# Kernel tuning notes

Measured on AMD Instinct MI355X. Metric: run time of the kernel, lower is better.

Reference implementation:

```python
import jax, jax.numpy as jnp
import numpy as np

N, C, H, W = 8, 128, 40, 40
EMBED, HEADS = 128, 8
HEAD_DIM = EMBED // HEADS  # 16


def setup_inputs() -> dict:
    key = jax.random.key(0)
    k1, k2, k3 = jax.random.split(key, 3)
    x = jax.random.normal(k1, (N, C, H, W), dtype=jnp.float32)
    # 1x1 conv weights collapsed to matrices
    w_qkv = jax.random.normal(k2, (3 * EMBED, C), dtype=jnp.float32) * (1.0 / np.sqrt(C))
    w_o = jax.random.normal(k3, (C, EMBED), dtype=jnp.float32) * (1.0 / np.sqrt(EMBED))
    b_o = jnp.zeros((C,), dtype=jnp.float32)
    return {"x": x, "w_qkv": w_qkv, "w_o": w_o, "b_o": b_o}


def reference(x, w_qkv, w_o, b_o):
    n, c, h, w = x.shape
    s = h * w  # spatial tokens
    # qkv 1x1 conv: (n, 3*embed, h, w) -> (n, heads, 3, head_dim, s)
    qkv = jnp.einsum('nchw,oc->nohw', x, w_qkv)
    qkv = qkv.reshape(n, HEADS, 3, HEAD_DIM, s)
    q, k, v = qkv[:, :, 0], qkv[:, :, 1], qkv[:, :, 2]  # (n, heads, head_dim, s)
    scale = 1.0 / jnp.sqrt(jnp.asarray(HEAD_DIM, dtype=x.dtype))
    # energy[n,h,i,j] = sum_c q[n,h,c,i] * k[n,h,c,j]
    energy = jnp.einsum('nhci,nhcj->nhij', q, k) * scale
    attn = jax.nn.softmax(energy, axis=-1)  # (n, heads, s, s)
    # out[n,h,c,i] = sum_j attn[n,h,i,j] * v[n,h,c,j]
    out = jnp.einsum('nhij,nhcj->nhci', attn, v)
    out = out.reshape(n, HEADS * HEAD_DIM, h, w)
    o = jnp.einsum('nchw,oc->nohw', out, w_o) + b_o[None, :, None, None]
    return o
```

## Files before the change

kernel.cpp:

```cpp
#include <hip/hip_runtime.h>
#include <hip/hip_bf16.h>

#define NB    8
#define CIN   128
#define SLEN  1600
#define HEADS 8
#define HD    16
#define NH    64
#define VCH   17

#define QKV_SUB (NH * HD * SLEN)
#define VB_SUB  (NH * VCH * SLEN)

#define SCALE_Q 0.36067376022224085f

typedef __attribute__((ext_vector_type(8)))  short  short8;
typedef __attribute__((ext_vector_type(16))) float  f32x16;
typedef __attribute__((ext_vector_type(2)))  unsigned uint2v;

__device__ inline unsigned short f2bf(float f) {
    union { float f; unsigned u; } x; x.f = f;
    unsigned r = x.u + 0x7FFFu + ((x.u >> 16) & 1u);
    return (unsigned short)(r >> 16);
}

__device__ inline unsigned pkbf(float a, float b) {
    __hip_bfloat162 h = __float22bfloat162_rn(make_float2(a, b));
    union { __hip_bfloat162 h; unsigned u; } c; c.h = h; return c.u;
}

__device__ inline short8 mk8(unsigned w0, unsigned w1, unsigned w2, unsigned w3) {
    union { unsigned u[4]; short8 s; } t;
    t.u[0] = w0; t.u[1] = w1; t.u[2] = w2; t.u[3] = w3; return t.s;
}

template <int MODE>
__global__ __launch_bounds__(256) void proj_kernel(const float* __restrict__ In,
                                                   const float* __restrict__ W,
                                                   const float* __restrict__ bias,
                                                   float* __restrict__ OutF,
                                                   unsigned short* __restrict__ qT,
                                                   unsigned short* __restrict__ kT,
                                                   unsigned short* __restrict__ vB) {
    __shared__ float Wt[128 * 64];
    __shared__ float Xt[128 * 64];

    const int tid = threadIdx.x;
    const int tx = tid & 15;
    const int ty = tid >> 4;
    const int n = blockIdx.z;
    const int m0 = blockIdx.y * 64;
    const int s0 = blockIdx.x * 64;

    const float4* W4 = (const float4*)W;
#pragma unroll
    for (int it = 0; it < 8; ++it) {
        int idx = tid + it * 256;
        int m = idx & 63;
        int k4 = idx >> 6;
        float4 wv = W4[(m0 + m) * 32 + k4];
        Wt[(k4 * 4 + 0) * 64 + m] = wv.x;
        Wt[(k4 * 4 + 1) * 64 + m] = wv.y;
        Wt[(k4 * 4 + 2) * 64 + m] = wv.z;
        Wt[(k4 * 4 + 3) * 64 + m] = wv.w;
    }
    const float4* X4 = (const float4*)In;
    float4* Xt4 = (float4*)Xt;
#pragma unroll
    for (int it = 0; it < 8; ++it) {
        int idx = tid + it * 256;
        int k = idx >> 4;
        int s4 = idx & 15;
        Xt4[k * 16 + s4] = X4[(n * CIN + k) * 400 + (s0 >> 2) + s4];
    }
    __syncthreads();

    const float4* Wt4 = (const float4*)Wt;
    const float4* Xt4r = (const float4*)Xt;
    float acc[4][4];
#pragma unroll
    for (int i = 0; i < 4; ++i)
#pragma unroll
        for (int j = 0; j < 4; ++j) acc[i][j] = 0.f;

#pragma unroll 4
    for (int k = 0; k < 128; ++k) {
        float4 a = Wt4[k * 16 + ty];
        float4 b = Xt4r[k * 16 + tx];
        float af[4] = {a.x, a.y, a.z, a.w};
        float bf[4] = {b.x, b.y, b.z, b.w};
#pragma unroll
        for (int i = 0; i < 4; ++i)
#pragma unroll
            for (int j = 0; j < 4; ++j) acc[i][j] += af[i] * bf[j];
    }

    if (MODE == 0) {
        int m = m0 + ty * 4;
        int h = m / 48;
        int r = m - h * 48;
        int which = r >> 4;
        int c0 = r & 15;
        int nh = n * HEADS + h;
        if (which == 2) {
#pragma unroll
            for (int i = 0; i < 4; ++i) {
                ushort4 w;
                w.x = f2bf(acc[i][0]); w.y = f2bf(acc[i][1]);
                w.z = f2bf(acc[i][2]); w.w = f2bf(acc[i][3]);
                *(ushort4*)(vB + (nh * VCH + c0 + i) * SLEN + s0 + tx * 4) = w;
            }
        } else {
            const float sc = (which == 0) ? SCALE_Q : 1.0f;
            unsigned short* base = (which == 0 ? qT : kT) + nh * (SLEN * HD);
#pragma unroll
            for (int j = 0; j < 4; ++j) {
                ushort4 w;
                w.x = f2bf(acc[0][j] * sc); w.y = f2bf(acc[1][j] * sc);
                w.z = f2bf(acc[2][j] * sc); w.w = f2bf(acc[3][j] * sc);
                *(ushort4*)(base + (s0 + tx * 4 + j) * HD + c0) = w;
            }
        }
        if (blockIdx.y == 0 && tid < 128) {
            int h2 = tid >> 4, s4 = tid & 15;
            ushort4 ones; ones.x = ones.y = ones.z = ones.w = 0x3F80;
            *(ushort4*)(vB + ((n * HEADS + h2) * VCH + 16) * SLEN + s0 + s4 * 4) = ones;
        }
    } else {
#pragma unroll
        for (int i = 0; i < 4; ++i) {
            int m = m0 + ty * 4 + i;
            float b = bias[m];
            float4 v;
            v.x = acc[i][0] + b; v.y = acc[i][1] + b;
            v.z = acc[i][2] + b; v.w = acc[i][3] + b;
            *(float4*)(OutF + (n * CIN + m) * SLEN + s0 + tx * 4) = v;
        }
    }
}

__global__ __launch_bounds__(64) void attn_mfma(const unsigned short* __restrict__ qT,
                                                const unsigned short* __restrict__ kT,
                                                const unsigned short* __restrict__ vB,
                                                float* __restrict__ ab) {
    const int lane = threadIdx.x;
    const int l31 = lane & 31, g = lane >> 5;
    const int nh = blockIdx.y;
    const int i0 = blockIdx.x * 32;

    const unsigned short* qbase = qT + nh * (SLEN * HD);
    const unsigned short* kptr = kT + nh * (SLEN * HD) + l31 * HD + g * 8;
    const unsigned short* vptr = vB + nh * (VCH * SLEN) + l31 * SLEN + g * 8;

    short8 qf = *(const short8*)(qbase + (i0 + l31) * HD + g * 8);

    f32x16 zz;
#pragma unroll
    for (int e = 0; e < 16; ++e) zz[e] = 0.f;
    f32x16 ov = zz;

    short8 k1 = *(const short8*)kptr;
    short8 vA0 = *(const short8*)vptr;
    short8 vB0 = *(const short8*)(vptr + 16);
    f32x16 sC = __builtin_amdgcn_mfma_f32_32x32x16_bf16(k1, qf, zz, 0, 0, 0);
    k1 = *(const short8*)(kptr + 32 * HD);
    short8 vA1 = *(const short8*)(vptr + 32);
    short8 vB1 = *(const short8*)(vptr + 48);
    const unsigned short* kp2 = kptr + 64 * HD;
    const unsigned short* vp2 = vptr + 64;

    for (int js = 0; js < 50; ++js) {
        short8 k2  = *(const short8*)kp2;
        short8 vA2 = *(const short8*)vp2;
        short8 vB2 = *(const short8*)(vp2 + 16);
        kp2 += 32 * HD; vp2 += 32;

        f32x16 sN = __builtin_amdgcn_mfma_f32_32x32x16_bf16(k1, qf, zz, 0, 0, 0);

        float p[16];
#pragma unroll
        for (int r = 0; r < 16; ++r) p[r] = __builtin_amdgcn_exp2f(sC[r]);

        unsigned P01 = pkbf(p[0], p[1]),   P23 = pkbf(p[2], p[3]);
        unsigned P45 = pkbf(p[4], p[5]),   P67 = pkbf(p[6], p[7]);
        unsigned P89 = pkbf(p[8], p[9]),   P1011 = pkbf(p[10], p[11]);
        unsigned P1213 = pkbf(p[12], p[13]), P1415 = pkbf(p[14], p[15]);

        uint2v s1 = __builtin_amdgcn_permlane32_swap(P01,   P45,   false, false);
        uint2v s2 = __builtin_amdgcn_permlane32_swap(P23,   P67,   false, false);
        uint2v s3 = __builtin_amdgcn_permlane32_swap(P89,   P1213, false, false);
        uint2v s4 = __builtin_amdgcn_permlane32_swap(P1011, P1415, false, false);
        short8 A1 = mk8(s1[0], s2[0], s1[1], s2[1]);
        short8 A2 = mk8(s3[0], s4[0], s3[1], s4[1]);

        ov = __builtin_amdgcn_mfma_f32_32x32x16_bf16(A1, vA0, ov, 0, 0, 0);
        ov = __builtin_amdgcn_mfma_f32_32x32x16_bf16(A2, vB0, ov, 0, 0, 0);

        sC = sN;
        k1 = k2; vA0 = vA1; vB0 = vB1; vA1 = vA2; vB1 = vB2;
    }

    const int src = 16 + (lane & 32);
    float* obase = ab + (nh * HD + l31) * SLEN + i0;
#pragma unroll
    for (int q = 0; q < 4; ++q) {
        float r0 = __shfl(ov[4 * q + 0], src);
        float r1 = __shfl(ov[4 * q + 1], src);
        float r2 = __shfl(ov[4 * q + 2], src);
        float r3 = __shfl(ov[4 * q + 3], src);
        if (l31 < 16) {
            float4 res;
            res.x = ov[4 * q + 0] / r0;
            res.y = ov[4 * q + 1] / r1;
            res.z = ov[4 * q + 2] / r2;
            res.w = ov[4 * q + 3] / r3;
            *(float4*)(obase + q * 8 + 4 * g) = res;
        }
    }
}

extern "C" void kernel_launch(void* const* d_in, const int* in_sizes, int n_in,
                              void* d_out, int out_size, void* d_ws, size_t ws_size,
                              hipStream_t stream) {
    const float* x     = (const float*)d_in[0];
    const float* w_qkv = (const float*)d_in[1];
    const float* w_o   = (const float*)d_in[2];
    const float* b_o   = (const float*)d_in[3];
    float* out = (float*)d_out;

    unsigned short* qT = (unsigned short*)d_ws;
    unsigned short* kT = qT + QKV_SUB;
    unsigned short* vB = kT + QKV_SUB;
    float* ab = (float*)(vB + VB_SUB);

    proj_kernel<0><<<dim3(25, 6, NB), 256, 0, stream>>>(x, w_qkv, nullptr, nullptr, qT, kT, vB);
    attn_mfma<<<dim3(50, NH), 64, 0, stream>>>(qT, kT, vB, ab);
    proj_kernel<1><<<dim3(25, 2, NB), 256, 0, stream>>>(ab, w_o, b_o, out, nullptr, nullptr, nullptr);
}
```

Measured before the change: 144.3 us.

## Replace FP32 projection GEMMs with bf16 MFMA GEMMs via transposed cast pre-pass

Adds a cast kernel that converts x to bf16 in a token-major layout and converts both weight matrices to bf16. The QKV and output projections then run as 32x32x16 bf16 MFMA GEMMs that read operands straight from global memory, replacing the FP32 shared-memory SIMT GEMMs. The attention kernel now writes its normalized output as bf16 in token-major layout so the output GEMM can consume it directly. This adds one extra kernel launch, extra precision loss in x and the weights, and strided scalar stores in the GEMM epilogues.

```diff
diff --git a/kernel.cpp b/kernel.cpp
--- a/kernel.cpp
+++ b/kernel.cpp
@@ -9,8 +9,11 @@
 #define NH    64
 #define VCH   17
 
-#define QKV_SUB (NH * HD * SLEN)
-#define VB_SUB  (NH * VCH * SLEN)
+#define XT_SUB   (NB * SLEN * CIN)
+#define WQ_SUB   (3 * CIN * CIN)
+#define WO_SUB   (CIN * CIN)
+#define QKV_SUB  (NH * HD * SLEN)
+#define VB_SUB   (NH * VCH * SLEN)
 
 #define SCALE_Q 0.36067376022224085f
 
@@ -34,115 +37,164 @@
     t.u[0] = w0; t.u[1] = w1; t.u[2] = w2; t.u[3] = w3; return t.s;
 }
 
-template <int MODE>
-__global__ __launch_bounds__(256) void proj_kernel(const float* __restrict__ In,
-                                                   const float* __restrict__ W,
-                                                   const float* __restrict__ bias,
-                                                   float* __restrict__ OutF,
-                                                   unsigned short* __restrict__ qT,
-                                                   unsigned short* __restrict__ kT,
-                                                   unsigned short* __restrict__ vB) {
-    __shared__ float Wt[128 * 64];
-    __shared__ float Xt[128 * 64];
-
+__global__ __launch_bounds__(64) void cast_kernel(const float* __restrict__ x,
+                                                  const float* __restrict__ w_qkv,
+                                                  const float* __restrict__ w_o,
+                                                  unsigned short* __restrict__ xT,
+                                                  unsigned short* __restrict__ wq,
+                                                  unsigned short* __restrict__ wo) {
+    const int lane = threadIdx.x;
+    const int bx = blockIdx.x;
+    const int n = blockIdx.y;
+    if (bx < 25) {
+        const int s = bx * 64 + lane;
+        const float* xp = x + n * (CIN * SLEN) + s;
+        unsigned short* op = xT + (n * SLEN + s) * CIN;
+#pragma unroll 4
+        for (int c0 = 0; c0 < CIN; c0 += 8) {
+            float v[8];
+#pragma unroll
+            for (int u = 0; u < 8; ++u) v[u] = xp[(c0 + u) * SLEN];
+            union { unsigned short us[8]; uint4 u4; } t;
+#pragma unroll
+            for (int u = 0; u < 8; ++u) t.us[u] = f2bf(v[u]);
+            *(uint4*)(op + c0) = t.u4;
+        }
+    } else if (n < 2) {
+        const float* src = (n == 0) ? w_qkv : w_o;
+        unsigned short* dst = (n == 0) ? wq : wo;
+        const int cnt = (n == 0) ? WQ_SUB : WO_SUB;
+        for (int i = lane * 4; i < cnt; i += 64 * 4) {
+            float4 v = *(const float4*)(src + i);
+            ushort4 w;
+            w.x = f2bf(v.x); w.y = f2bf(v.y); w.z = f2bf(v.z); w.w = f2bf(v.w);
+            *(ushort4*)(dst + i) = w;
+        }
+    }
+}
+
+__global__ __launch_bounds__(384) void qkv_gemm(const unsigned short* __restrict__ xT,
+                                                const unsigned short* __restrict__ wq,
+                                                unsigned short* __restrict__ qT,
+                                                unsigned short* __restrict__ kT,
+                                                unsigned short* __restrict__ vB) {
     const int tid = threadIdx.x;
-    const int tx = tid & 15;
-    const int ty = tid >> 4;
-    const int n = blockIdx.z;
-    const int m0 = blockIdx.y * 64;
+    const int wave = tid >> 6;
+    const int lane = tid & 63;
+    const int l31 = lane & 31, g = lane >> 5;
+    const int n = blockIdx.y;
     const int s0 = blockIdx.x * 64;
-
-    const float4* W4 = (const float4*)W;
-#pragma unroll
-    for (int it = 0; it < 8; ++it) {
-        int idx = tid + it * 256;
-        int m = idx & 63;
-        int k4 = idx >> 6;
-        float4 wv = W4[(m0 + m) * 32 + k4];
-        Wt[(k4 * 4 + 0) * 64 + m] = wv.x;
-        Wt[(k4 * 4 + 1) * 64 + m] = wv.y;
-        Wt[(k4 * 4 + 2) * 64 + m] = wv.z;
-        Wt[(k4 * 4 + 3) * 64 + m] = wv.w;
-    }
-    const float4* X4 = (const float4*)In;
-    float4* Xt4 = (float4*)Xt;
-#pragma unroll
-    for (int it = 0; it < 8; ++it) {
-        int idx = tid + it * 256;
-        int k = idx >> 4;
-        int s4 = idx & 15;
-        Xt4[k * 16 + s4] = X4[(n * CIN + k) * 400 + (s0 >> 2) + s4];
-    }
-    __syncthreads();
-
-    const float4* Wt4 = (const float4*)Wt;
-    const float4* Xt4r = (const float4*)Xt;
-    float acc[4][4];
-#pragma unroll
-    for (int i = 0; i < 4; ++i)
-#pragma unroll
-        for (int j = 0; j < 4; ++j) acc[i][j] = 0.f;
-
-#pragma unroll 4
-    for (int k = 0; k < 128; ++k) {
-        float4 a = Wt4[k * 16 + ty];
-        float4 b = Xt4r[k * 16 + tx];
-        float af[4] = {a.x, a.y, a.z, a.w};
-        float bf[4] = {b.x, b.y, b.z, b.w};
-#pragma unroll
-        for (int i = 0; i < 4; ++i)
-#pragma unroll
-            for (int j = 0; j < 4; ++j) acc[i][j] += af[i] * bf[j];
-    }
-
-    if (MODE == 0) {
-        int m = m0 + ty * 4;
-        int h = m / 48;
-        int r = m - h * 48;
-        int which = r >> 4;
-        int c0 = r & 15;
-        int nh = n * HEADS + h;
-        if (which == 2) {
-#pragma unroll
-            for (int i = 0; i < 4; ++i) {
-                ushort4 w;
-                w.x = f2bf(acc[i][0]); w.y = f2bf(acc[i][1]);
-                w.z = f2bf(acc[i][2]); w.w = f2bf(acc[i][3]);
-                *(ushort4*)(vB + (nh * VCH + c0 + i) * SLEN + s0 + tx * 4) = w;
+    const int m0 = wave * 64;
+
+    const unsigned short* Ab = wq + (m0 + l31) * CIN + g * 8;
+    const unsigned short* Bb = xT + (n * SLEN + s0 + l31) * CIN + g * 8;
+
+    f32x16 acc00, acc01, acc10, acc11;
+#pragma unroll
+    for (int e = 0; e < 16; ++e) { acc00[e] = 0.f; acc01[e] = 0.f; acc10[e] = 0.f; acc11[e] = 0.f; }
+
+#pragma unroll
+    for (int ks = 0; ks < 8; ++ks) {
+        short8 A0 = *(const short8*)(Ab + ks * 16);
+        short8 A1 = *(const short8*)(Ab + 32 * CIN + ks * 16);
+        short8 B0 = *(const short8*)(Bb + ks * 16);
+        short8 B1 = *(const short8*)(Bb + 32 * CIN + ks * 16);
+        acc00 = __builtin_amdgcn_mfma_f32_32x32x16_bf16(A0, B0, acc00, 0, 0, 0);
+        acc01 = __builtin_amdgcn_mfma_f32_32x32x16_bf16(A0, B1, acc01, 0, 0, 0);
+        acc10 = __builtin_amdgcn_mfma_f32_32x32x16_bf16(A1, B0, acc10, 0, 0, 0);
+        acc11 = __builtin_amdgcn_mfma_f32_32x32x16_bf16(A1, B1, acc11, 0, 0, 0);
+    }
+
+#pragma unroll
+    for (int mt = 0; mt < 2; ++mt)
+#pragma unroll
+        for (int st = 0; st < 2; ++st) {
+            f32x16 a = mt ? (st ? acc11 : acc10) : (st ? acc01 : acc00);
+            const int s = s0 + st * 32 + l31;
+#pragma unroll
+            for (int q = 0; q < 4; ++q) {
+                int mb = m0 + mt * 32 + 8 * q + 4 * g;
+                int h = mb / 48;
+                int r48 = mb - h * 48;
+                int which = r48 >> 4;
+                int c0 = r48 & 15;
+                int nh = n * HEADS + h;
+                if (which == 2) {
+#pragma unroll
+                    for (int e = 0; e < 4; ++e)
+                        vB[(nh * VCH + c0 + e) * SLEN + s] = f2bf(a[4 * q + e]);
+                } else {
+                    const float sc = (which == 0) ? SCALE_Q : 1.0f;
+                    unsigned short* dst = ((which == 0) ? qT : kT) + nh * (SLEN * HD) + s * HD + c0;
+                    ushort4 w;
+                    w.x = f2bf(a[4 * q + 0] * sc); w.y = f2bf(a[4 * q + 1] * sc);
+                    w.z = f2bf(a[4 * q + 2] * sc); w.w = f2bf(a[4 * q + 3] * sc);
+                    *(ushort4*)dst = w;
+                }
             }
-        } else {
-            const float sc = (which == 0) ? SCALE_Q : 1.0f;
-            unsigned short* base = (which == 0 ? qT : kT) + nh * (SLEN * HD);
-#pragma unroll
-            for (int j = 0; j < 4; ++j) {
-                ushort4 w;
-                w.x = f2bf(acc[0][j] * sc); w.y = f2bf(acc[1][j] * sc);
-                w.z = f2bf(acc[2][j] * sc); w.w = f2bf(acc[3][j] * sc);
-                *(ushort4*)(base + (s0 + tx * 4 + j) * HD + c0) = w;
+        }
+
+    if (wave == 0) {
+        int s = s0 + lane;
+#pragma unroll
+        for (int h = 0; h < HEADS; ++h)
+            vB[((n * HEADS + h) * VCH + 16) * SLEN + s] = 0x3F80;
+    }
+}
+
+__global__ __launch_bounds__(128) void out_gemm(const unsigned short* __restrict__ abT,
+                                                const unsigned short* __restrict__ wo,
+                                                const float* __restrict__ bias,
+                                                float* __restrict__ out) {
+    const int tid = threadIdx.x;
+    const int wave = tid >> 6;
+    const int lane = tid & 63;
+    const int l31 = lane & 31, g = lane >> 5;
+    const int n = blockIdx.y;
+    const int s0 = blockIdx.x * 64;
+    const int m0 = wave * 64;
+
+    const unsigned short* Ab = wo + (m0 + l31) * CIN + g * 8;
+    const unsigned short* Bb = abT + (n * SLEN + s0 + l31) * CIN + g * 8;
+
+    f32x16 acc00, acc01, acc10, acc11;
+#pragma unroll
+    for (int e = 0; e < 16; ++e) { acc00[e] = 0.f; acc01[e] = 0.f; acc10[e] = 0.f; acc11[e] = 0.f; }
+
+#pragma unroll
+    for (int ks = 0; ks < 8; ++ks) {
+        short8 A0 = *(const short8*)(Ab + ks * 16);
+        short8 A1 = *(const short8*)(Ab + 32 * CIN + ks * 16);
+        short8 B0 = *(const short8*)(Bb + ks * 16);
+        short8 B1 = *(const short8*)(Bb + 32 * CIN + ks * 16);
+        acc00 = __builtin_amdgcn_mfma_f32_32x32x16_bf16(A0, B0, acc00, 0, 0, 0);
+        acc01 = __builtin_amdgcn_mfma_f32_32x32x16_bf16(A0, B1, acc01, 0, 0, 0);
+        acc10 = __builtin_amdgcn_mfma_f32_32x32x16_bf16(A1, B0, acc10, 0, 0, 0);
+        acc11 = __builtin_amdgcn_mfma_f32_32x32x16_bf16(A1, B1, acc11, 0, 0, 0);
+    }
+
+#pragma unroll
+    for (int mt = 0; mt < 2; ++mt)
+#pragma unroll
+        for (int st = 0; st < 2; ++st) {
+            f32x16 a = mt ? (st ? acc11 : acc10) : (st ? acc01 : acc00);
+            const int s = s0 + st * 32 + l31;
+#pragma unroll
+            for (int q = 0; q < 4; ++q) {
+                int mb = m0 + mt * 32 + 8 * q + 4 * g;
+                float4 b = *(const float4*)(bias + mb);
+                out[(n * CIN + mb + 0) * SLEN + s] = a[4 * q + 0] + b.x;
+                out[(n * CIN + mb + 1) * SLEN + s] = a[4 * q + 1] + b.y;
+                out[(n * CIN + mb + 2) * SLEN + s] = a[4 * q + 2] + b.z;
+                out[(n * CIN + mb + 3) * SLEN + s] = a[4 * q + 3] + b.w;
             }
         }
-        if (blockIdx.y == 0 && tid < 128) {
-            int h2 = tid >> 4, s4 = tid & 15;
-            ushort4 ones; ones.x = ones.y = ones.z = ones.w = 0x3F80;
-            *(ushort4*)(vB + ((n * HEADS + h2) * VCH + 16) * SLEN + s0 + s4 * 4) = ones;
-        }
-    } else {
-#pragma unroll
-        for (int i = 0; i < 4; ++i) {
-            int m = m0 + ty * 4 + i;
-            float b = bias[m];
-            float4 v;
-            v.x = acc[i][0] + b; v.y = acc[i][1] + b;
-            v.z = acc[i][2] + b; v.w = acc[i][3] + b;
-            *(float4*)(OutF + (n * CIN + m) * SLEN + s0 + tx * 4) = v;
-        }
-    }
 }
 
 __global__ __launch_bounds__(64) void attn_mfma(const unsigned short* __restrict__ qT,
                                                 const unsigned short* __restrict__ kT,
                                                 const unsigned short* __restrict__ vB,
-                                                float* __restrict__ ab) {
+                                                unsigned short* __restrict__ abT) {
     const int lane = threadIdx.x;
     const int l31 = lane & 31, g = lane >> 5;
     const int nh = blockIdx.y;
@@ -201,20 +253,13 @@
     }
 
     const int src = 16 + (lane & 32);
-    float* obase = ab + (nh * HD + l31) * SLEN + i0;
-#pragma unroll
-    for (int q = 0; q < 4; ++q) {
-        float r0 = __shfl(ov[4 * q + 0], src);
-        float r1 = __shfl(ov[4 * q + 1], src);
-        float r2 = __shfl(ov[4 * q + 2], src);
-        float r3 = __shfl(ov[4 * q + 3], src);
+    const int nb = nh >> 3, h = nh & 7;
+#pragma unroll
+    for (int e = 0; e < 16; ++e) {
+        float r = __shfl(ov[e], src);
         if (l31 < 16) {
-            float4 res;
-            res.x = ov[4 * q + 0] / r0;
-            res.y = ov[4 * q + 1] / r1;
-            res.z = ov[4 * q + 2] / r2;
-            res.w = ov[4 * q + 3] / r3;
-            *(float4*)(obase + q * 8 + 4 * g) = res;
+            int i = (e & 3) + 8 * (e >> 2) + 4 * g;
+            abT[(nb * SLEN + i0 + i) * CIN + h * HD + l31] = f2bf(ov[e] / r);
         }
     }
 }
@@ -228,12 +273,16 @@
     const float* b_o   = (const float*)d_in[3];
     float* out = (float*)d_out;
 
-    unsigned short* qT = (unsigned short*)d_ws;
-    unsigned short* kT = qT + QKV_SUB;
-    unsigned short* vB = kT + QKV_SUB;
-    float* ab = (float*)(vB + VB_SUB);
-
-    proj_kernel<0><<<dim3(25, 6, NB), 256, 0, stream>>>(x, w_qkv, nullptr, nullptr, qT, kT, vB);
-    attn_mfma<<<dim3(50, NH), 64, 0, stream>>>(qT, kT, vB, ab);
-    proj_kernel<1><<<dim3(25, 2, NB), 256, 0, stream>>>(ab, w_o, b_o, out, nullptr, nullptr, nullptr);
-}
+    unsigned short* xT  = (unsigned short*)d_ws;
+    unsigned short* wq  = xT + XT_SUB;
+    unsigned short* wo  = wq + WQ_SUB;
+    unsigned short* qT  = wo + WO_SUB;
+    unsigned short* kT  = qT + QKV_SUB;
+    unsigned short* vB  = kT + QKV_SUB;
+    unsigned short* abT = vB + VB_SUB;
+
+    cast_kernel<<<dim3(26, NB), 64, 0, stream>>>(x, w_qkv, w_o, xT, wq, wo);
+    qkv_gemm<<<dim3(25, NB), 384, 0, stream>>>(xT, wq, qT, kT, vB);
+    attn_mfma<<<dim3(50, NH), 64, 0, stream>>>(qT, kT, vB, abT);
+    out_gemm<<<dim3(25, NB), 128, 0, stream>>>(abT, wo, b_o, out);
+}
```

Result: slower. 158.3 us (+9.7%).
